# Optimization experiments

Hardware: AMD Instinct MI355X
Metric: run time of the kernel (lower is better)

Reference implementation:

```python
import jax, jax.numpy as jnp
import numpy as np

N = 100000
E = 1600000
F_IN = 256   # 4 * 64 after concat
H = 128

def _glorot(key, shape):
    fan_in, fan_out = shape
    lim = jnp.sqrt(6.0 / (fan_in + fan_out))
    return jax.random.uniform(key, shape, jnp.float32, -lim, lim)

def setup_inputs() -> dict:
    key = jax.random.key(0)
    ks = jax.random.split(key, 32)
    inp = {
        'x': jax.random.normal(ks[0], (N, 64), jnp.float32),
        'diff': jax.random.normal(ks[1], (N, 64), jnp.float32),
        'rec_prev': jax.random.normal(ks[2], (N, 64), jnp.float32),
        'hidden_prev': jax.random.normal(ks[3], (N, 64), jnp.float32),
        'edge_index': jax.random.randint(ks[4], (2, E), 0, N, jnp.int64),
    }
    dims = [(F_IN, H), (H, H), (H, H), (H, 1)]
    for i, (din, dout) in enumerate(dims):
        inp[f'Wl{i}'] = _glorot(ks[5 + 3 * i], (din, dout))  # neighbor (aggr) weight
        inp[f'Wr{i}'] = _glorot(ks[6 + 3 * i], (din, dout))  # root weight
        inp[f'b{i}'] = jnp.zeros((dout,), jnp.float32)
    return inp

def _sage_conv(h, src, dst, Wl, Wr, b):
    # mean aggregation of source-node features at destination nodes (PyG SAGEConv)
    msg_sum = jax.ops.segment_sum(h[src], dst, num_segments=N)        # [N, F]
    cnt = jax.ops.segment_sum(jnp.ones((src.shape[0],), h.dtype), dst, num_segments=N)
    mean = msg_sum / jnp.maximum(cnt, 1.0)[:, None]
    return mean @ Wl + h @ Wr + b

def reference(x, diff, rec_prev, hidden_prev, edge_index,
              Wl0, Wr0, b0, Wl1, Wr1, b1, Wl2, Wr2, b2, Wl3, Wr3, b3):
    src, dst = edge_index[0], edge_index[1]
    h = jnp.concatenate([x, diff, rec_prev, hidden_prev], axis=1)  # [N, 256]
    params = [(Wl0, Wr0, b0), (Wl1, Wr1, b1), (Wl2, Wr2, b2), (Wl3, Wr3, b3)]
    h = _sage_conv(h, src, dst, *params[0])
    for Wl, Wr, b in params[1:]:
        h = jax.nn.relu(h)
        h = _sage_conv(h, src, dst, Wl, Wr, b)
    out = jax.nn.sigmoid(h)          # [N, 1]
    lwp_util = jnp.mean(out)
    return out, lwp_util
```

## Files before the change

### kernel.cpp

```cpp
#include <hip/hip_runtime.h>
#include <hip/hip_bf16.h>

#define NN 100000
#define EE 1600000
#define HH 128
#define NB 391
#define CAP 5120
#define GB 1563

typedef short bf16x8 __attribute__((ext_vector_type(8)));
typedef short bf16x4 __attribute__((ext_vector_type(4)));
typedef float f32x4  __attribute__((ext_vector_type(4)));

__device__ inline short f2bf(float v) {
    __hip_bfloat16 b = __float2bfloat16(v);
    return *reinterpret_cast<short*>(&b);
}

__global__ __launch_bounds__(1024) void prep_kernel(
    const float* __restrict__ Wl0, const float* __restrict__ Wr0,
    const float* __restrict__ Wl1, const float* __restrict__ Wr1,
    const float* __restrict__ Wl2, const float* __restrict__ Wr2,
    __hip_bfloat16* __restrict__ WT0, __hip_bfloat16* __restrict__ WT1,
    __hip_bfloat16* __restrict__ WT2, int* __restrict__ bcur) {
    const int t = threadIdx.x;
    if (blockIdx.x == 128) {
        if (t < NB) bcur[t] = 0;
        return;
    }
    int id = blockIdx.x * 1024 + t;
    if (id < 65536) {
        int k = id & 255, n = id >> 8;
        float v = (n < 128) ? Wl0[(size_t)k * 128 + n]
                            : Wr0[(size_t)k * 128 + (n - 128)];
        WT0[(size_t)n * 256 + k] = __float2bfloat16(v);
    } else {
        id -= 65536;
        int layer = id >> 15;
        int u = id & 32767;
        int k = u & 127, n = u >> 7;
        const float* Wl = layer ? Wl2 : Wl1;
        const float* Wr = layer ? Wr2 : Wr1;
        __hip_bfloat16* WT = layer ? WT2 : WT1;
        float v = (n < 128) ? Wl[(size_t)k * 128 + n]
                            : Wr[(size_t)k * 128 + (n - 128)];
        WT[(size_t)n * 128 + k] = __float2bfloat16(v);
    }
}

#define TSW 152
template <int K, bool FIRST>
__device__ __forceinline__ void gemm_body(
    short* __restrict__ lsh, int bid,
    const __hip_bfloat16* hin,
    const float* __restrict__ x0, const float* __restrict__ x1,
    const float* __restrict__ x2, const float* __restrict__ x3,
    const __hip_bfloat16* __restrict__ wt, const float* __restrict__ bias,
    __hip_bfloat16* zout, __hip_bfloat16* __restrict__ rout) {
    const int t    = threadIdx.x;
    const int w    = t >> 6;
    const int lane = t & 63;
    const int quad = lane >> 4;
    const int l16  = lane & 15;
    const int n0   = bid * 64;

    const __hip_bfloat16* afeat[4];
#pragma unroll
    for (int ft = 0; ft < 4; ++ft)
        afeat[ft] = wt + (size_t)(w * 64 + ft * 16 + l16) * K + quad * 8;

    f32x4 acc[4][4];
#pragma unroll
    for (int ft = 0; ft < 4; ++ft)
#pragma unroll
        for (int nt = 0; nt < 4; ++nt)
            acc[ft][nt] = (f32x4){0.f, 0.f, 0.f, 0.f};

    constexpr int NPASS = K / 128;
#pragma unroll
    for (int pass = 0; pass < NPASS; ++pass) {
        if (FIRST) {
            const float* sA = pass ? x2 : x0;
            const float* sB = pass ? x3 : x1;
#pragma unroll
            for (int u = 0; u < 8; ++u) {
                const int id  = u * 256 + t;
                const int row = id >> 5, c4 = (id & 31) * 4;
                int rg = n0 + row; if (rg > NN - 1) rg = NN - 1;
                const float* s = (c4 < 64) ? sA : sB;
                const float4 v = *(const float4*)&s[(size_t)rg * 64 + (c4 & 63)];
                bf16x4 p;
                p[0] = f2bf(v.x); p[1] = f2bf(v.y);
                p[2] = f2bf(v.z); p[3] = f2bf(v.w);
                *(bf16x4*)&lsh[row * TSW + c4] = p;
            }
        } else {
#pragma unroll
            for (int u = 0; u < 4; ++u) {
                const int id  = u * 256 + t;
                const int row = id >> 4, c8 = (id & 15) * 8;
                int rg = n0 + row; if (rg > NN - 1) rg = NN - 1;
                const bf16x8 v = *(const bf16x8*)&hin[(size_t)rg * K + c8];
                *(bf16x8*)&lsh[row * TSW + c8] = v;
            }
        }
        __syncthreads();

#pragma unroll
        for (int kcl = 0; kcl < 4; ++kcl) {
            const int kc = pass * 4 + kcl;
            bf16x8 af[4];
#pragma unroll
            for (int ft = 0; ft < 4; ++ft)
                af[ft] = *(const bf16x8*)(afeat[ft] + kc * 32);
            bf16x8 bf[4];
#pragma unroll
            for (int nt = 0; nt < 4; ++nt)
                bf[nt] = *(const bf16x8*)&lsh[(nt * 16 + l16) * TSW + kcl * 32 + quad * 8];
#pragma unroll
            for (int ft = 0; ft < 4; ++ft)
#pragma unroll
                for (int nt = 0; nt < 4; ++nt)
                    acc[ft][nt] = __builtin_amdgcn_mfma_f32_16x16x32_bf16(
                        af[ft], bf[nt], acc[ft][nt], 0, 0, 0);
        }
        __syncthreads();
    }

    if (w < 2) {
#pragma unroll
        for (int ft = 0; ft < 4; ++ft) {
            const int fb = ft * 16 + quad * 4;
#pragma unroll
            for (int nt = 0; nt < 4; ++nt) {
                const f32x4 a = acc[ft][nt];
                bf16x4 p;
                p[0] = f2bf(a[0]); p[1] = f2bf(a[1]);
                p[2] = f2bf(a[2]); p[3] = f2bf(a[3]);
                *(bf16x4*)&lsh[(nt * 16 + l16) * TSW + w * 64 + fb] = p;
            }
        }
    }
    __syncthreads();
#pragma unroll
    for (int u = 0; u < 4; ++u) {
        const int id  = u * 256 + t;
        const int row = id >> 4, ch = (id & 15) * 8;
        const int nd  = n0 + row;
        if (nd < NN)
            *(bf16x8*)&zout[(size_t)nd * HH + ch] = *(const bf16x8*)&lsh[row * TSW + ch];
    }
    __syncthreads();

    if (w >= 2) {
        const int fcol = (w - 2) * 64;
#pragma unroll
        for (int ft = 0; ft < 4; ++ft) {
            const int fb = ft * 16 + quad * 4;
            const float4 bv = *(const float4*)&bias[fcol + fb];
#pragma unroll
            for (int nt = 0; nt < 4; ++nt) {
                const f32x4 a = acc[ft][nt];
                bf16x4 p;
                p[0] = f2bf(a[0] + bv.x); p[1] = f2bf(a[1] + bv.y);
                p[2] = f2bf(a[2] + bv.z); p[3] = f2bf(a[3] + bv.w);
                *(bf16x4*)&lsh[(nt * 16 + l16) * TSW + fcol + fb] = p;
            }
        }
    }
    __syncthreads();
#pragma unroll
    for (int u = 0; u < 4; ++u) {
        const int id  = u * 256 + t;
        const int row = id >> 4, ch = (id & 15) * 8;
        const int nd  = n0 + row;
        if (nd < NN)
            *(bf16x8*)&rout[(size_t)nd * HH + ch] = *(const bf16x8*)&lsh[row * TSW + ch];
    }
}

template <int K, bool FIRST>
__global__ __launch_bounds__(256) void gemm_kernel(
    const __hip_bfloat16* hin,
    const float* __restrict__ x0, const float* __restrict__ x1,
    const float* __restrict__ x2, const float* __restrict__ x3,
    const __hip_bfloat16* __restrict__ wt, const float* __restrict__ bias,
    __hip_bfloat16* zout, __hip_bfloat16* __restrict__ rout) {
    __shared__ short lsh[64 * TSW];
    gemm_body<K, FIRST>(lsh, blockIdx.x, hin, x0, x1, x2, x3, wt, bias, zout, rout);
}

__global__ __launch_bounds__(256) void gemm0_scatter_kernel(
    const float* __restrict__ x0, const float* __restrict__ x1,
    const float* __restrict__ x2, const float* __restrict__ x3,
    const __hip_bfloat16* __restrict__ wt, const float* __restrict__ bias,
    __hip_bfloat16* __restrict__ zout, __hip_bfloat16* __restrict__ rout,
    const int* __restrict__ srcv, const int* __restrict__ dstv,
    int* __restrict__ bcur, int* __restrict__ pairs) {
    __shared__ short lsh[64 * TSW];
    const int t = threadIdx.x;

    if (blockIdx.x < GB) {
        gemm_body<256, true>(lsh, blockIdx.x, nullptr, x0, x1, x2, x3,
                             wt, bias, zout, rout);
        return;
    }

    int* hist = (int*)lsh;
    int* base = hist + NB;
    for (int j = t; j < NB; j += 256) hist[j] = 0;
    __syncthreads();

    const int e0 = (blockIdx.x - GB) * 4096;
    int s[16], d[16];
#pragma unroll
    for (int u = 0; u < 16; ++u) {
        const int e = e0 + u * 256 + t;
        if (e < EE) {
            s[u] = srcv[e]; d[u] = dstv[e];
            atomicAdd(&hist[d[u] >> 8], 1);
        } else {
            d[u] = -1;
        }
    }
    __syncthreads();

    for (int j = t; j < NB; j += 256)
        base[j] = hist[j] ? atomicAdd(&bcur[j], hist[j]) : 0;
    __syncthreads();
    for (int j = t; j < NB; j += 256) hist[j] = base[j];
    __syncthreads();

#pragma unroll
    for (int u = 0; u < 16; ++u)
        if (d[u] >= 0) {
            const int b   = d[u] >> 8;
            const int pos = atomicAdd(&hist[b], 1);
            if (pos < CAP) pairs[b * CAP + pos] = (s[u] << 8) | (d[u] & 255);
        }
}

__global__ __launch_bounds__(256) void finalize_kernel(
    const int* __restrict__ bcur, const int* __restrict__ pairs,
    int* __restrict__ csr, int* __restrict__ beg, int* __restrict__ eend,
    float* __restrict__ inv) {
    __shared__ int cnt[256];
    __shared__ int scn[256];
    __shared__ int cur[256];
    const int b = blockIdx.x, t = threadIdx.x;
    int m = bcur[b];
    if (m > CAP) m = CAP;

    cnt[t] = 0;
    __syncthreads();
    for (int e = t; e < m; e += 256)
        atomicAdd(&cnt[pairs[b * CAP + e] & 255], 1);
    __syncthreads();

    const int v = cnt[t];
    scn[t] = v;
    __syncthreads();
    for (int st = 1; st < 256; st <<= 1) {
        int tv = (t >= st) ? scn[t - st] : 0;
        __syncthreads();
        scn[t] += tv;
        __syncthreads();
    }
    const int myStart = scn[t] - v;
    cur[t] = myStart;
    __syncthreads();

    for (int e = t; e < m; e += 256) {
        const int pk  = pairs[b * CAP + e];
        const int pos = atomicAdd(&cur[pk & 255], 1);
        csr[b * CAP + pos] = pk >> 8;
    }

    const int node = b * 256 + t;
    if (node < NN) {
        beg[node]  = b * CAP + myStart;
        eend[node] = b * CAP + myStart + v;
        inv[node]  = 1.0f / fmaxf((float)v, 1.0f);
    }
}

template <bool LAST>
__global__ __launch_bounds__(256) void aggregate_kernel(
    const __hip_bfloat16* __restrict__ z, __hip_bfloat16* __restrict__ rio,
    const int* __restrict__ beg, const int* __restrict__ eend,
    const int* __restrict__ csr, const float* __restrict__ inv,
    const float* __restrict__ Wl3, const float* __restrict__ Wr3,
    const float* __restrict__ b3, float* __restrict__ z3,
    float* __restrict__ r3) {
    const int i    = (blockIdx.x * 256 + threadIdx.x) >> 6;
    const int lane = threadIdx.x & 63;
    const int g    = lane >> 4;
    const int l16  = lane & 15;
    if (i >= NN) return;
    const int b0 = beg[i], e0 = eend[i];

    float acc[8];
#pragma unroll
    for (int j = 0; j < 8; ++j) acc[j] = 0.f;

    int e = b0 + g;
    for (; e + 12 < e0; e += 16) {
        const int s0 = csr[e];
        const int s1 = csr[e + 4];
        const int s2 = csr[e + 8];
        const int s3 = csr[e + 12];
        const bf16x8 z0 = *(const bf16x8*)&z[(size_t)s0 * HH + l16 * 8];
        const bf16x8 z1 = *(const bf16x8*)&z[(size_t)s1 * HH + l16 * 8];
        const bf16x8 z2 = *(const bf16x8*)&z[(size_t)s2 * HH + l16 * 8];
        const bf16x8 z3v = *(const bf16x8*)&z[(size_t)s3 * HH + l16 * 8];
        const __hip_bfloat162* p0 = (const __hip_bfloat162*)&z0;
        const __hip_bfloat162* p1 = (const __hip_bfloat162*)&z1;
        const __hip_bfloat162* p2 = (const __hip_bfloat162*)&z2;
        const __hip_bfloat162* p3 = (const __hip_bfloat162*)&z3v;
#pragma unroll
        for (int j = 0; j < 4; ++j) {
            acc[2 * j]     += __bfloat162float(p0[j].x) + __bfloat162float(p1[j].x)
                            + __bfloat162float(p2[j].x) + __bfloat162float(p3[j].x);
            acc[2 * j + 1] += __bfloat162float(p0[j].y) + __bfloat162float(p1[j].y)
                            + __bfloat162float(p2[j].y) + __bfloat162float(p3[j].y);
        }
    }
    for (; e < e0; e += 4) {
        const int s0 = csr[e];
        const bf16x8 z0 = *(const bf16x8*)&z[(size_t)s0 * HH + l16 * 8];
        const __hip_bfloat162* p0 = (const __hip_bfloat162*)&z0;
#pragma unroll
        for (int j = 0; j < 4; ++j) {
            acc[2 * j]     += __bfloat162float(p0[j].x);
            acc[2 * j + 1] += __bfloat162float(p0[j].y);
        }
    }

#pragma unroll
    for (int j = 0; j < 8; ++j) {
        acc[j] += __shfl_xor(acc[j], 16, 64);
        acc[j] += __shfl_xor(acc[j], 32, 64);
    }

    const float iv = inv[i];
    const int   f  = l16 * 8 + g * 2;
    const __hip_bfloat162 rv = *(const __hip_bfloat162*)&rio[(size_t)i * HH + f];
    const float ox = fmaxf(acc[g * 2]     * iv + __bfloat162float(rv.x), 0.f);
    const float oy = fmaxf(acc[g * 2 + 1] * iv + __bfloat162float(rv.y), 0.f);

    if (!LAST) {
        __hip_bfloat162 o;
        o.x = __float2bfloat16(ox);
        o.y = __float2bfloat16(oy);
        *(__hip_bfloat162*)&rio[(size_t)i * HH + f] = o;
    } else {
        const float2 wl = *(const float2*)&Wl3[f];
        const float2 wr = *(const float2*)&Wr3[f];
        float al = ox * wl.x + oy * wl.y;
        float ar = ox * wr.x + oy * wr.y;
#pragma unroll
        for (int m = 32; m; m >>= 1) {
            al += __shfl_xor(al, m, 64);
            ar += __shfl_xor(ar, m, 64);
        }
        if (lane == 0) {
            z3[i] = al;
            r3[i] = ar + b3[0];
        }
    }
}

__global__ __launch_bounds__(256) void final_kernel(
    const float* __restrict__ z3, const float* __restrict__ r3,
    const int* __restrict__ beg, const int* __restrict__ eend,
    const int* __restrict__ csr, const float* __restrict__ inv,
    float* __restrict__ out, float* __restrict__ partial) {
    __shared__ float red[4];
    const int i    = (blockIdx.x * 256 + threadIdx.x) >> 6;
    const int lane = threadIdx.x & 63;
    const int w    = threadIdx.x >> 6;
    float v = 0.f;
    if (i < NN) {
        const int b0 = beg[i], e0 = eend[i];
        float a = 0.f;
        for (int e = b0 + lane; e < e0; e += 64) a += z3[csr[e]];
#pragma unroll
        for (int m = 32; m; m >>= 1) a += __shfl_xor(a, m, 64);
        const float pre = a * inv[i] + r3[i];
        const float s = 1.f / (1.f + __expf(-pre));
        if (lane == 0) { out[i] = s; v = s; }
    }
    if (lane == 0) red[w] = v;
    __syncthreads();
    if (threadIdx.x == 0)
        partial[blockIdx.x] = red[0] + red[1] + red[2] + red[3];
}

__global__ __launch_bounds__(256) void mean_kernel(const float* __restrict__ partial,
                                                   int nb, float* __restrict__ out) {
    __shared__ float lds[256];
    float s = 0.f;
    for (int i = threadIdx.x; i < nb; i += 256) s += partial[i];
    lds[threadIdx.x] = s;
    __syncthreads();
    for (int st = 128; st; st >>= 1) {
        if (threadIdx.x < st) lds[threadIdx.x] += lds[threadIdx.x + st];
        __syncthreads();
    }
    if (threadIdx.x == 0) out[NN] = lds[0] / (float)NN;
}

extern "C" void kernel_launch(void* const* d_in, const int* in_sizes, int n_in,
                              void* d_out, int out_size, void* d_ws, size_t ws_size,
                              hipStream_t stream) {
    const float* x    = (const float*)d_in[0];
    const float* diff = (const float*)d_in[1];
    const float* rec  = (const float*)d_in[2];
    const float* hid  = (const float*)d_in[3];
    const int* edge   = (const int*)d_in[4];
    const int* esrc = edge;
    const int* edst = edge + EE;
    const float* Wl0 = (const float*)d_in[5];
    const float* Wr0 = (const float*)d_in[6];
    const float* b0  = (const float*)d_in[7];
    const float* Wl1 = (const float*)d_in[8];
    const float* Wr1 = (const float*)d_in[9];
    const float* b1  = (const float*)d_in[10];
    const float* Wl2 = (const float*)d_in[11];
    const float* Wr2 = (const float*)d_in[12];
    const float* b2  = (const float*)d_in[13];
    const float* Wl3 = (const float*)d_in[14];
    const float* Wr3 = (const float*)d_in[15];
    const float* b3  = (const float*)d_in[16];
    float* out = (float*)d_out;

    char* w = (char*)d_ws;
    auto alloc = [&](size_t bytes) -> void* {
        void* p = (void*)w;
        w += (bytes + 255) & ~(size_t)255;
        return p;
    };
    __hip_bfloat16* bufA = (__hip_bfloat16*)alloc((size_t)NN * HH * 2);
    __hip_bfloat16* bufB = (__hip_bfloat16*)alloc((size_t)NN * HH * 2);
    __hip_bfloat16* WT0  = (__hip_bfloat16*)alloc((size_t)256 * 256 * 2);
    __hip_bfloat16* WT1  = (__hip_bfloat16*)alloc((size_t)256 * 128 * 2);
    __hip_bfloat16* WT2  = (__hip_bfloat16*)alloc((size_t)256 * 128 * 2);
    int*   pairs   = (int*)alloc((size_t)NB * CAP * 4);
    int*   csr     = (int*)alloc((size_t)NB * CAP * 4);
    int*   bcur    = (int*)alloc((size_t)512 * 4);
    int*   beg     = (int*)alloc((size_t)NN * 4);
    int*   eend    = (int*)alloc((size_t)NN * 4);
    float* inv     = (float*)alloc((size_t)NN * 4);
    float* z3      = (float*)alloc((size_t)NN * 4);
    float* r3      = (float*)alloc((size_t)NN * 4);
    float* partial = (float*)alloc((size_t)25000 * 4);

    const int WB = (NN + 3) / 4;

    prep_kernel<<<129, 1024, 0, stream>>>(Wl0, Wr0, Wl1, Wr1, Wl2, Wr2,
                                          WT0, WT1, WT2, bcur);

    gemm0_scatter_kernel<<<GB + NB, 256, 0, stream>>>(
        x, diff, rec, hid, WT0, b0, bufA, bufB, esrc, edst, bcur, pairs);

    finalize_kernel<<<NB, 256, 0, stream>>>(bcur, pairs, csr, beg, eend, inv);

    aggregate_kernel<false><<<WB, 256, 0, stream>>>(bufA, bufB, beg, eend, csr, inv,
                                                    nullptr, nullptr, nullptr,
                                                    nullptr, nullptr);

    gemm_kernel<128, false><<<GB, 256, 0, stream>>>(bufB, nullptr, nullptr, nullptr, nullptr,
                                                    WT1, b1, bufB, bufA);
    aggregate_kernel<false><<<WB, 256, 0, stream>>>(bufB, bufA, beg, eend, csr, inv,
                                                    nullptr, nullptr, nullptr,
                                                    nullptr, nullptr);

    gemm_kernel<128, false><<<GB, 256, 0, stream>>>(bufA, nullptr, nullptr, nullptr, nullptr,
                                                    WT2, b2, bufA, bufB);
    aggregate_kernel<true><<<WB, 256, 0, stream>>>(bufA, bufB, beg, eend, csr, inv,
                                                   Wl3, Wr3, b3, z3, r3);

    final_kernel<<<WB, 256, 0, stream>>>(z3, r3, beg, eend, csr, inv, out, partial);
    mean_kernel<<<1, 256, 0, stream>>>(partial, WB, out);
}
```

Baseline: 513.4 us.

## Double-buffer GEMM activation tiles with async global-to-LDS loads and swizzle

```diff
diff --git a/kernel.cpp b/kernel.cpp
--- a/kernel.cpp
+++ b/kernel.cpp
@@ -15,6 +15,18 @@
 __device__ inline short f2bf(float v) {
     __hip_bfloat16 b = __float2bfloat16(v);
     return *reinterpret_cast<short*>(&b);
+}
+
+typedef __attribute__((address_space(1))) void gvoid_t;
+typedef __attribute__((address_space(3))) void svoid_t;
+__device__ __forceinline__ void gload16(const void* g, void* l) {
+    __builtin_amdgcn_global_load_lds((gvoid_t*)g, (svoid_t*)l, 16, 0, 0);
+}
+
+__device__ __forceinline__ void waitbar(int n) {
+    if (n == 0)      asm volatile("s_waitcnt vmcnt(0)\n\ts_barrier" ::: "memory");
+    else if (n == 2) asm volatile("s_waitcnt vmcnt(2)\n\ts_barrier" ::: "memory");
+    else             asm volatile("s_waitcnt vmcnt(4)\n\ts_barrier" ::: "memory");
 }
 
 __global__ __launch_bounds__(1024) void prep_kernel(
@@ -64,6 +76,11 @@
     const int l16  = lane & 15;
     const int n0   = bid * 64;
 
+    constexpr int NS   = K / 64;
+    constexpr int BUFB = FIRST ? 16384 : 8192;
+    constexpr int GPW  = FIRST ? 4 : 2;
+    char* const lc = (char*)lsh;
+
     const __hip_bfloat16* afeat[4];
 #pragma unroll
     for (int ft = 0; ft < 4; ++ft)
@@ -76,55 +93,75 @@
         for (int nt = 0; nt < 4; ++nt)
             acc[ft][nt] = (f32x4){0.f, 0.f, 0.f, 0.f};
 
-    constexpr int NPASS = K / 128;
-#pragma unroll
-    for (int pass = 0; pass < NPASS; ++pass) {
-        if (FIRST) {
-            const float* sA = pass ? x2 : x0;
-            const float* sB = pass ? x3 : x1;
-#pragma unroll
-            for (int u = 0; u < 8; ++u) {
-                const int id  = u * 256 + t;
-                const int row = id >> 5, c4 = (id & 31) * 4;
+    auto stage = [&](int p, int bb) {
+        char* lb = lc + bb * BUFB;
+        if constexpr (FIRST) {
+            const float* sp = (p == 0) ? x0 : (p == 1) ? x1 : (p == 2) ? x2 : x3;
+#pragma unroll
+            for (int i = 0; i < 4; ++i) {
+                const int j   = w * 4 + i;
+                const int row = j * 4 + (lane >> 4);
                 int rg = n0 + row; if (rg > NN - 1) rg = NN - 1;
-                const float* s = (c4 < 64) ? sA : sB;
-                const float4 v = *(const float4*)&s[(size_t)rg * 64 + (c4 & 63)];
-                bf16x4 p;
-                p[0] = f2bf(v.x); p[1] = f2bf(v.y);
-                p[2] = f2bf(v.z); p[3] = f2bf(v.w);
-                *(bf16x4*)&lsh[row * TSW + c4] = p;
+                const int colb = ((lane & 15) * 16) ^ ((row & 15) << 4);
+                gload16((const char*)sp + (size_t)rg * 256 + colb, lb + j * 1024);
             }
         } else {
 #pragma unroll
-            for (int u = 0; u < 4; ++u) {
-                const int id  = u * 256 + t;
-                const int row = id >> 4, c8 = (id & 15) * 8;
+            for (int i = 0; i < 2; ++i) {
+                const int j   = w * 2 + i;
+                const int row = j * 8 + (lane >> 3);
                 int rg = n0 + row; if (rg > NN - 1) rg = NN - 1;
-                const bf16x8 v = *(const bf16x8*)&hin[(size_t)rg * K + c8];
-                *(bf16x8*)&lsh[row * TSW + c8] = v;
+                const int colb = ((lane & 7) * 16) ^ ((row & 7) << 4);
+                gload16((const char*)hin + (size_t)rg * 256 + p * 128 + colb,
+                        lb + j * 1024);
             }
         }
-        __syncthreads();
-
-#pragma unroll
-        for (int kcl = 0; kcl < 4; ++kcl) {
-            const int kc = pass * 4 + kcl;
+    };
+
+    auto compute = [&](int s) {
+        const char* lb = lc + (s & 1) * BUFB;
+#pragma unroll
+        for (int kcl = 0; kcl < 2; ++kcl) {
+            const int kc = s * 2 + kcl;
             bf16x8 af[4];
 #pragma unroll
             for (int ft = 0; ft < 4; ++ft)
                 af[ft] = *(const bf16x8*)(afeat[ft] + kc * 32);
-            bf16x8 bf[4];
-#pragma unroll
-            for (int nt = 0; nt < 4; ++nt)
-                bf[nt] = *(const bf16x8*)&lsh[(nt * 16 + l16) * TSW + kcl * 32 + quad * 8];
-#pragma unroll
-            for (int ft = 0; ft < 4; ++ft)
-#pragma unroll
-                for (int nt = 0; nt < 4; ++nt)
+#pragma unroll
+            for (int nt = 0; nt < 4; ++nt) {
+                const int row = nt * 16 + l16;
+                bf16x8 b;
+                if constexpr (FIRST) {
+                    const int sw = (row & 15) << 4;
+                    const int B0 = kcl * 128 + quad * 32;
+                    const char* rb = lb + row * 256;
+                    const f32x4 lo = *(const f32x4*)(rb + ((B0) ^ sw));
+                    const f32x4 hi = *(const f32x4*)(rb + ((B0 + 16) ^ sw));
+                    b[0] = f2bf(lo[0]); b[1] = f2bf(lo[1]);
+                    b[2] = f2bf(lo[2]); b[3] = f2bf(lo[3]);
+                    b[4] = f2bf(hi[0]); b[5] = f2bf(hi[1]);
+                    b[6] = f2bf(hi[2]); b[7] = f2bf(hi[3]);
+                } else {
+                    const int sw = (row & 7) << 4;
+                    const int B0 = kcl * 64 + quad * 16;
+                    b = *(const bf16x8*)(lb + row * 128 + (B0 ^ sw));
+                }
+#pragma unroll
+                for (int ft = 0; ft < 4; ++ft)
                     acc[ft][nt] = __builtin_amdgcn_mfma_f32_16x16x32_bf16(
-                        af[ft], bf[nt], acc[ft][nt], 0, 0, 0);
-        }
-        __syncthreads();
+                        af[ft], b, acc[ft][nt], 0, 0, 0);
+            }
+        }
+    };
+
+    stage(0, 0);
+    stage(1, 1);
+#pragma unroll
+    for (int s = 0; s < NS; ++s) {
+        waitbar(s < NS - 1 ? GPW : 0);
+        compute(s);
+        asm volatile("s_barrier" ::: "memory");
+        if (s + 2 < NS) stage(s + 2, s & 1);
     }
 
     if (w < 2) {
@@ -186,7 +223,7 @@
     const float* __restrict__ x2, const float* __restrict__ x3,
     const __hip_bfloat16* __restrict__ wt, const float* __restrict__ bias,
     __hip_bfloat16* zout, __hip_bfloat16* __restrict__ rout) {
-    __shared__ short lsh[64 * TSW];
+    __shared__ short lsh[9728];
     gemm_body<K, FIRST>(lsh, blockIdx.x, hin, x0, x1, x2, x3, wt, bias, zout, rout);
 }
 
@@ -197,11 +234,11 @@
     __hip_bfloat16* __restrict__ zout, __hip_bfloat16* __restrict__ rout,
     const int* __restrict__ srcv, const int* __restrict__ dstv,
     int* __restrict__ bcur, int* __restrict__ pairs) {
-    __shared__ short lsh[64 * TSW];
+    __shared__ short lsh[16384];
     const int t = threadIdx.x;
 
-    if (blockIdx.x < GB) {
-        gemm_body<256, true>(lsh, blockIdx.x, nullptr, x0, x1, x2, x3,
+    if (blockIdx.x >= NB) {
+        gemm_body<256, true>(lsh, blockIdx.x - NB, nullptr, x0, x1, x2, x3,
                              wt, bias, zout, rout);
         return;
     }
@@ -211,7 +248,7 @@
     for (int j = t; j < NB; j += 256) hist[j] = 0;
     __syncthreads();
 
-    const int e0 = (blockIdx.x - GB) * 4096;
+    const int e0 = blockIdx.x * 4096;
     int s[16], d[16];
 #pragma unroll
     for (int u = 0; u < 16; ++u) {
```

Measured after the change: 500.0 us. -2.6%, faster.
